# Kernel tuning notes

Measured on AMD Instinct MI355X. Metric: run time of the kernel, lower is better.

## Reference

```python
import jax, jax.numpy as jnp
import numpy as np

B, S, E, H = 8, 1024, 512, 8
NEG = -1e10


def setup_inputs() -> dict:
    key = jax.random.key(0)
    ks = jax.random.split(key, 8)
    k = jax.random.normal(ks[0], (B, S, E), dtype=jnp.float32)
    v = jax.random.normal(ks[1], (B, S, E), dtype=jnp.float32)
    q = jax.random.normal(ks[2], (B, S, E), dtype=jnp.float32)
    # causal mask, broadcastable like torch masked_fill
    mask = jnp.tril(jnp.ones((S, S), dtype=jnp.int32))[None, None]
    sc = 1.0 / np.sqrt(E)
    Wk = jax.random.normal(ks[3], (H * E, E), dtype=jnp.float32) * sc
    Wq = jax.random.normal(ks[4], (H * E, E), dtype=jnp.float32) * sc
    Wv = jax.random.normal(ks[5], (H * E, E), dtype=jnp.float32) * sc
    Wo = jax.random.normal(ks[6], (E, H * E), dtype=jnp.float32) * (1.0 / np.sqrt(H * E))
    bo = jnp.zeros((E,), dtype=jnp.float32)
    return {"k": k, "v": v, "q": q, "mask": mask,
            "Wk": Wk, "Wq": Wq, "Wv": Wv, "Wo": Wo, "bo": bo}


def reference(k, v, q, mask, Wk, Wq, Wv, Wo, bo):
    b, q_len, e = q.shape
    k_len, v_len = k.shape[1], v.shape[1]
    h = Wk.shape[0] // e
    scale = jnp.sqrt(jnp.asarray(e // h, dtype=jnp.float32))
    # projections E -> H*E (torch Linear: x @ W.T)
    wk = (k @ Wk.T).reshape(b, h, k_len, e)   # raw reshape, matches torch .view
    wq = (q @ Wq.T).reshape(b, h, q_len, e)
    wv = (v @ Wv.T).reshape(b, h, v_len, e)
    energy = jnp.einsum('bhqe,bhke->bhqk', wq, wk)
    energy = jnp.where(mask == 0, NEG, energy)  # mask applied BEFORE scaling, as in source
    energy = energy / scale
    attn = jax.nn.softmax(energy, axis=-1)
    f = jnp.einsum('bhqk,bhke->bhqe', attn, wv)
    f = jnp.transpose(f, (0, 2, 1, 3)).reshape(b, q_len, h * e)
    return f @ Wo.T + bo
```

## Files before the change

### kernel.cpp

```cpp
#include <hip/hip_runtime.h>


typedef _Float16 half8 __attribute__((ext_vector_type(8)));
typedef _Float16 half4v __attribute__((ext_vector_type(4)));
typedef float f32x4 __attribute__((ext_vector_type(4)));

typedef __attribute__((address_space(3))) unsigned int lds_u32_t;
typedef __attribute__((address_space(1))) unsigned int g_u32_t;

__device__ __forceinline__ void glds16(const void* g, void* l) {
  __builtin_amdgcn_global_load_lds((const g_u32_t*)g, (lds_u32_t*)l, 16, 0, 0);
}

__device__ __forceinline__ void stage_glds(const _Float16* tile, int ld, _Float16* lds) {
  int w = (int)threadIdx.x >> 6, lane = (int)threadIdx.x & 63;
  int row = lane >> 2, seg = (lane & 3) * 8;
  const _Float16* g0 = tile + (size_t)(w * 32 + row) * ld + seg;
  const _Float16* g1 = tile + (size_t)(w * 32 + 16 + row) * ld + seg;
  glds16(g0, lds + (size_t)(w * 32) * 32);
  glds16(g1, lds + (size_t)(w * 32 + 16) * 32);
}

template <int C3, int CMODE, bool CAUSAL, bool KLIM, int HL>
__global__ __launch_bounds__(256) void gemm_bt(
    const _Float16* __restrict__ Ap, const _Float16* __restrict__ Bp,
    void* __restrict__ C0, void* __restrict__ C1, void* __restrict__ C2,
    int tilesN, int K, int lda, int ldb, int ldc,
    long sAy, long sAz, long sAh, long sBy, long sBz, long sBh,
    long sCy, long sCz) {
  int i0 = ((int)blockIdx.x / tilesN) * 128;
  int j0 = ((int)blockIdx.x % tilesN) * 128;
  if (CAUSAL && j0 > i0) return;
  int Y = (int)blockIdx.y, Z = (int)blockIdx.z;
  const _Float16* Ab = Ap + (size_t)Y * sAy + (size_t)Z * sAz + (size_t)i0 * lda;
  const _Float16* Bb = Bp + (size_t)Y * sBy + (size_t)Z * sBz + (size_t)j0 * ldb;
  void* Cb = C3 ? (Y == 0 ? C0 : (Y == 1 ? C1 : C2)) : C0;
  size_t cOff = (C3 ? 0 : (size_t)Y * sCy) + (size_t)Z * sCz;

  __shared__ __align__(16) _Float16 As[128 * 32];
  __shared__ __align__(16) _Float16 Bs[128 * 32];

  int kmax = K;
  if (KLIM) { int kl = i0 + 128; kmax = kl < K ? kl : K; }

  int w = (int)threadIdx.x >> 6;
  int lane = (int)threadIdx.x & 63;
  int wr = (w >> 1) * 64, wc = (w & 1) * 64;
  int lr = lane & 15, lk = (lane >> 4) * 8;

  f32x4 acc[4][4] = {};

  for (int h = 0; h < HL; h++) {
    const _Float16* At = Ab + (size_t)h * sAh;
    const _Float16* Bt = Bb + (size_t)h * sBh;
    for (int k0 = 0; k0 < kmax; k0 += 32) {
      __syncthreads();
      stage_glds(At + k0, lda, As);
      stage_glds(Bt + k0, ldb, Bs);
      __syncthreads();

      half8 a[4], b[4];
#pragma unroll
      for (int mi = 0; mi < 4; mi++)
        a[mi] = *(half8*)&As[(wr + mi * 16 + lr) * 32 + lk];
#pragma unroll
      for (int ni = 0; ni < 4; ni++)
        b[ni] = *(half8*)&Bs[(wc + ni * 16 + lr) * 32 + lk];
#pragma unroll
      for (int mi = 0; mi < 4; mi++)
#pragma unroll
        for (int ni = 0; ni < 4; ni++)
          acc[mi][ni] = __builtin_amdgcn_mfma_f32_16x16x32_f16(a[mi], b[ni], acc[mi][ni], 0, 0, 0);
    }
  }

  int r0 = (lane >> 4) * 4, col = lane & 15;
#pragma unroll
  for (int mi = 0; mi < 4; mi++) {
#pragma unroll
    for (int ni = 0; ni < 4; ni++) {
      int gcol = j0 + wc + ni * 16 + col;
      int growb = i0 + wr + mi * 16 + r0;
#pragma unroll
      for (int r = 0; r < 4; r++) {
        size_t off = cOff + (size_t)(growb + r) * ldc + gcol;
        if (CMODE == 1)
          unsafeAtomicAdd((float*)Cb + off, acc[mi][ni][r]);
        else
          ((_Float16*)Cb)[off] = (_Float16)acc[mi][ni][r];
      }
    }
  }
}

__global__ __launch_bounds__(256) void softmax_rows(void* __restrict__ Ep) {
  int R = (int)blockIdx.x * 4 + ((int)threadIdx.x >> 6);
  int lane = (int)threadIdx.x & 63;
  int i = R & 1023;
  int nt = (i >> 8) + 1;
  _Float16* row = (_Float16*)Ep + (size_t)R * 1024;
  float x[16];
  float m = -3.0e38f;
#pragma unroll
  for (int t = 0; t < 4; t++) {
    if (t < nt) {
      int j0 = t * 256 + lane * 4;
      half4v h = *(const half4v*)(row + j0);
#pragma unroll
      for (int c = 0; c < 4; c++) {
        float v = (j0 + c <= i) ? (float)h[c] * 0.125f : -3.0e38f;
        x[t * 4 + c] = v;
        m = fmaxf(m, v);
      }
    }
  }
#pragma unroll
  for (int s = 32; s > 0; s >>= 1) m = fmaxf(m, __shfl_xor(m, s, 64));
  float p[16];
  float sum = 0.0f;
#pragma unroll
  for (int t = 0; t < 4; t++) {
    if (t < nt) {
#pragma unroll
      for (int c = 0; c < 4; c++) {
        p[t * 4 + c] = exp2f((x[t * 4 + c] - m) * 1.44269504f);
        sum += p[t * 4 + c];
      }
    }
  }
#pragma unroll
  for (int s = 32; s > 0; s >>= 1) sum += __shfl_xor(sum, s, 64);
  float inv = 1.0f / sum;
#pragma unroll
  for (int t = 0; t < 4; t++) {
    if (t < nt) {
      int j0 = t * 256 + lane * 4;
      half4v h;
#pragma unroll
      for (int c = 0; c < 4; c++) h[c] = (_Float16)(p[t * 4 + c] * inv);
      *(half4v*)(row + j0) = h;
    }
  }
}

__global__ __launch_bounds__(256) void wconv(const float* __restrict__ Wq,
                                             const float* __restrict__ Wk,
                                             const float* __restrict__ Wv,
                                             const float* __restrict__ Wo,
                                             _Float16* __restrict__ W16) {
  size_t base = ((size_t)blockIdx.x * 256 + threadIdx.x) * 8;
  int wid = (int)(base >> 21);
  size_t off = base & 2097151;
  const float* src = wid == 0 ? Wq : (wid == 1 ? Wk : (wid == 2 ? Wv : Wo));
  float4 a = *(const float4*)(src + off);
  float4 b = *(const float4*)(src + off + 4);
  half8 h;
  h[0] = (_Float16)a.x; h[1] = (_Float16)a.y; h[2] = (_Float16)a.z; h[3] = (_Float16)a.w;
  h[4] = (_Float16)b.x; h[5] = (_Float16)b.y; h[6] = (_Float16)b.z; h[7] = (_Float16)b.w;
  *(half8*)(W16 + base) = h;
}

template <int HG>
__global__ __launch_bounds__(256) void inconv(const float* __restrict__ q,
                                              const float* __restrict__ k,
                                              const float* __restrict__ v,
                                              _Float16* __restrict__ dst) {
  int Y = (int)blockIdx.y;
  size_t base = ((size_t)blockIdx.x * 256 + threadIdx.x) * 8;
  size_t b = base / (HG * 65536);
  size_t within = base - b * (HG * 65536);
  const float* src = (Y == 0 ? q : (Y == 1 ? k : v)) + b * 524288 + within;
  float4 a = ((const float4*)src)[0];
  float4 c = ((const float4*)src)[1];
  half8 h;
  h[0] = (_Float16)a.x; h[1] = (_Float16)a.y; h[2] = (_Float16)a.z; h[3] = (_Float16)a.w;
  h[4] = (_Float16)c.x; h[5] = (_Float16)c.y; h[6] = (_Float16)c.z; h[7] = (_Float16)c.w;
  *(half8*)(dst + (size_t)Y * HG * 524288 + base) = h;
}

__global__ __launch_bounds__(256) void bias_init(float* __restrict__ out,
                                                 const float* __restrict__ bo) {
  size_t idx = ((size_t)blockIdx.x * 256 + threadIdx.x) * 4;
  *(float4*)(out + idx) = *(const float4*)(bo + (idx & 511));
}

template <int HG>
static void run_pipeline(const float* q_in, const float* k_in, const float* v_in,
                         const float* Wq, const float* Wk, const float* Wv,
                         const float* Wo, const float* bo, float* out, char* ws,
                         hipStream_t stream) {
  const int NG = 8 / HG;
  const long zc = 8 * HG;
  _Float16* W16 = (_Float16*)ws;
  _Float16* in16 = W16 + 8388608;
  _Float16* Qp = in16 + 3L * HG * 524288;
  _Float16* Kp = Qp + zc * 524288;
  _Float16* VWo = Kp + zc * 524288;
  _Float16* E = VWo + zc * 524288;
  _Float16* Vp = E;
  _Float16* Wo16 = W16 + 3 * 2097152;
  dim3 blk(256);

  wconv<<<dim3(4096), blk, 0, stream>>>(Wq, Wk, Wv, Wo, W16);
  bias_init<<<dim3(4096), blk, 0, stream>>>(out, bo);

  constexpr int YS = (HG > 1) ? HG / 2 : 1;
  constexpr int HL = HG / YS;

  for (int g = 0; g < NG; g++) {
    inconv<HG><<<dim3(HG * 256, 3), blk, 0, stream>>>(
        q_in + (size_t)g * HG * 65536, k_in + (size_t)g * HG * 65536,
        v_in + (size_t)g * HG * 65536, in16);

    gemm_bt<1, 0, false, false, 1><<<dim3(HG * 32, 3, 8), blk, 0, stream>>>(
        in16, W16, Qp, Kp, Vp, 32, 512, 512, 512, 4096,
        (long)HG * 524288, (long)HG * 65536, 0, 2097152, 0, 0,
        0, (long)HG * 524288);

    gemm_bt<0, 0, false, false, 1><<<dim3(32, HG, 8), blk, 0, stream>>>(
        Wo16 + (size_t)g * HG * 512, Vp, VWo, nullptr, nullptr,
        8, 512, 4096, 512, 1024,
        512, 0, 0, 524288, (long)HG * 524288, 0,
        524288, (long)HG * 524288);

    gemm_bt<0, 0, true, false, 1><<<dim3(64, HG, 8), blk, 0, stream>>>(
        Qp, Kp, E, nullptr, nullptr, 8, 512, 512, 512, 1024,
        524288, (long)HG * 524288, 0, 524288, (long)HG * 524288, 0,
        1048576, (long)HG * 1048576);

    softmax_rows<<<dim3(zc * 256), blk, 0, stream>>>(E);

    gemm_bt<0, 1, false, true, HL><<<dim3(32, YS, 8), blk, 0, stream>>>(
        E, VWo, out, nullptr, nullptr, 4, 1024, 1024, 1024, 512,
        (long)HL * 1048576, (long)HG * 1048576, 1048576,
        (long)HL * 524288, (long)HG * 524288, 524288,
        0, 524288);
  }
}

extern "C" void kernel_launch(void* const* d_in, const int* in_sizes, int n_in,
                              void* d_out, int out_size, void* d_ws, size_t ws_size,
                              hipStream_t stream) {
  const float* k_in = (const float*)d_in[0];
  const float* v_in = (const float*)d_in[1];
  const float* q_in = (const float*)d_in[2];
  const float* Wk = (const float*)d_in[4];
  const float* Wq = (const float*)d_in[5];
  const float* Wv = (const float*)d_in[6];
  const float* Wo = (const float*)d_in[7];
  const float* bo = (const float*)d_in[8];
  float* out = (float*)d_out;
  char* ws = (char*)d_ws;

  if (ws_size >= (size_t)197132288)
    run_pipeline<4>(q_in, k_in, v_in, Wq, Wk, Wv, Wo, bo, out, ws, stream);
  else if (ws_size >= (size_t)106954752)
    run_pipeline<2>(q_in, k_in, v_in, Wq, Wk, Wv, Wo, bo, out, ws, stream);
  else
    run_pipeline<1>(q_in, k_in, v_in, Wq, Wk, Wv, Wo, bo, out, ws, stream);
}
```

Before: 632.0 us.

## Split GEMM into specialized kernels with BK=64, LDS-staged stores, triangular causal grid

The generic gemm_bt is replaced by per-stage kernels built on a shared core that stages 64-wide K slices per barrier pair instead of 32. The f16 outputs now go through an LDS transpose so each thread writes 16-byte rows. The energy GEMM launches only the 36 lower-triangular tiles, computed with a sqrt index mapping, instead of returning early from masked blocks. The weight and bias init kernels merge into one launch, and the PV head split changes to HL=2. These aim to cut barrier count, scattered 2-byte stores and idle blocks, at the cost of more LDS per block, which may reduce occupancy.

```diff
diff --git a/kernel.cpp b/kernel.cpp
--- a/kernel.cpp
+++ b/kernel.cpp
@@ -12,85 +12,161 @@
   __builtin_amdgcn_global_load_lds((const g_u32_t*)g, (lds_u32_t*)l, 16, 0, 0);
 }
 
-__device__ __forceinline__ void stage_glds(const _Float16* tile, int ld, _Float16* lds) {
-  int w = (int)threadIdx.x >> 6, lane = (int)threadIdx.x & 63;
-  int row = lane >> 2, seg = (lane & 3) * 8;
-  const _Float16* g0 = tile + (size_t)(w * 32 + row) * ld + seg;
-  const _Float16* g1 = tile + (size_t)(w * 32 + 16 + row) * ld + seg;
-  glds16(g0, lds + (size_t)(w * 32) * 32);
-  glds16(g1, lds + (size_t)(w * 32 + 16) * 32);
-}
-
-template <int C3, int CMODE, bool CAUSAL, bool KLIM, int HL>
-__global__ __launch_bounds__(256) void gemm_bt(
-    const _Float16* __restrict__ Ap, const _Float16* __restrict__ Bp,
-    void* __restrict__ C0, void* __restrict__ C1, void* __restrict__ C2,
-    int tilesN, int K, int lda, int ldb, int ldc,
-    long sAy, long sAz, long sAh, long sBy, long sBz, long sBh,
-    long sCy, long sCz) {
-  int i0 = ((int)blockIdx.x / tilesN) * 128;
-  int j0 = ((int)blockIdx.x % tilesN) * 128;
-  if (CAUSAL && j0 > i0) return;
-  int Y = (int)blockIdx.y, Z = (int)blockIdx.z;
-  const _Float16* Ab = Ap + (size_t)Y * sAy + (size_t)Z * sAz + (size_t)i0 * lda;
-  const _Float16* Bb = Bp + (size_t)Y * sBy + (size_t)Z * sBz + (size_t)j0 * ldb;
-  void* Cb = C3 ? (Y == 0 ? C0 : (Y == 1 ? C1 : C2)) : C0;
-  size_t cOff = (C3 ? 0 : (size_t)Y * sCy) + (size_t)Z * sCz;
-
-  __shared__ __align__(16) _Float16 As[128 * 32];
-  __shared__ __align__(16) _Float16 Bs[128 * 32];
-
-  int kmax = K;
-  if (KLIM) { int kl = i0 + 128; kmax = kl < K ? kl : K; }
-
-  int w = (int)threadIdx.x >> 6;
-  int lane = (int)threadIdx.x & 63;
+template <int HL>
+__device__ __forceinline__ void gemm_core(const _Float16* A, const _Float16* B,
+                                          int lda, int ldb, int kmax,
+                                          long sAh, long sBh,
+                                          _Float16* As, _Float16* Bs,
+                                          f32x4 (&acc)[4][4]) {
+  int tid = (int)threadIdx.x;
+  int w = tid >> 6, lane = tid & 63;
   int wr = (w >> 1) * 64, wc = (w & 1) * 64;
   int lr = lane & 15, lk = (lane >> 4) * 8;
-
-  f32x4 acc[4][4] = {};
+  int srow = lane >> 2, sseg = (lane & 3) * 8;
 
   for (int h = 0; h < HL; h++) {
-    const _Float16* At = Ab + (size_t)h * sAh;
-    const _Float16* Bt = Bb + (size_t)h * sBh;
-    for (int k0 = 0; k0 < kmax; k0 += 32) {
+    const _Float16* Ah = A + (size_t)h * sAh;
+    const _Float16* Bh = B + (size_t)h * sBh;
+    for (int k0 = 0; k0 < kmax; k0 += 64) {
       __syncthreads();
-      stage_glds(At + k0, lda, As);
-      stage_glds(Bt + k0, ldb, Bs);
+#pragma unroll
+      for (int p = 0; p < 2; p++)
+#pragma unroll
+        for (int t = 0; t < 2; t++) {
+          glds16(Ah + (size_t)(w * 32 + t * 16 + srow) * lda + k0 + p * 32 + sseg,
+                 As + p * 4096 + (w * 32 + t * 16) * 32);
+          glds16(Bh + (size_t)(w * 32 + t * 16 + srow) * ldb + k0 + p * 32 + sseg,
+                 Bs + p * 4096 + (w * 32 + t * 16) * 32);
+        }
       __syncthreads();
-
-      half8 a[4], b[4];
-#pragma unroll
-      for (int mi = 0; mi < 4; mi++)
-        a[mi] = *(half8*)&As[(wr + mi * 16 + lr) * 32 + lk];
-#pragma unroll
-      for (int ni = 0; ni < 4; ni++)
-        b[ni] = *(half8*)&Bs[(wc + ni * 16 + lr) * 32 + lk];
-#pragma unroll
-      for (int mi = 0; mi < 4; mi++)
+#pragma unroll
+      for (int p = 0; p < 2; p++) {
+        half8 a[4], b[4];
+#pragma unroll
+        for (int mi = 0; mi < 4; mi++)
+          a[mi] = *(half8*)&As[p * 4096 + (wr + mi * 16 + lr) * 32 + lk];
 #pragma unroll
         for (int ni = 0; ni < 4; ni++)
-          acc[mi][ni] = __builtin_amdgcn_mfma_f32_16x16x32_f16(a[mi], b[ni], acc[mi][ni], 0, 0, 0);
-    }
-  }
-
-  int r0 = (lane >> 4) * 4, col = lane & 15;
-#pragma unroll
-  for (int mi = 0; mi < 4; mi++) {
-#pragma unroll
-    for (int ni = 0; ni < 4; ni++) {
-      int gcol = j0 + wc + ni * 16 + col;
-      int growb = i0 + wr + mi * 16 + r0;
-#pragma unroll
-      for (int r = 0; r < 4; r++) {
-        size_t off = cOff + (size_t)(growb + r) * ldc + gcol;
-        if (CMODE == 1)
-          unsafeAtomicAdd((float*)Cb + off, acc[mi][ni][r]);
-        else
-          ((_Float16*)Cb)[off] = (_Float16)acc[mi][ni][r];
+          b[ni] = *(half8*)&Bs[p * 4096 + (wc + ni * 16 + lr) * 32 + lk];
+#pragma unroll
+        for (int mi = 0; mi < 4; mi++)
+#pragma unroll
+          for (int ni = 0; ni < 4; ni++)
+            acc[mi][ni] =
+                __builtin_amdgcn_mfma_f32_16x16x32_f16(a[mi], b[ni], acc[mi][ni], 0, 0, 0);
       }
     }
   }
+}
+
+__device__ __forceinline__ void epilogue_f16(f32x4 (&acc)[4][4], _Float16* T,
+                                             _Float16* Cp, size_t cOff,
+                                             int i0, int j0, int ldc) {
+  int tid = (int)threadIdx.x;
+  int w = tid >> 6, lane = tid & 63;
+  int wr = (w >> 1) * 64, wc = (w & 1) * 64;
+  int r0 = (lane >> 4) * 4, col = lane & 15;
+  __syncthreads();
+#pragma unroll
+  for (int mi = 0; mi < 4; mi++)
+#pragma unroll
+    for (int ni = 0; ni < 4; ni++)
+#pragma unroll
+      for (int r = 0; r < 4; r++)
+        T[(size_t)(wr + mi * 16 + r0 + r) * 136 + wc + ni * 16 + col] =
+            (_Float16)acc[mi][ni][r];
+  __syncthreads();
+#pragma unroll
+  for (int s = 0; s < 8; s++) {
+    int row = w * 32 + s * 4 + (lane >> 4);
+    int c8 = (lane & 15) * 8;
+    half8 h = *(half8*)&T[(size_t)row * 136 + c8];
+    *(half8*)(Cp + cOff + (size_t)(i0 + row) * ldc + j0 + c8) = h;
+  }
+}
+
+__device__ __forceinline__ void epilogue_atomic(f32x4 (&acc)[4][4], float* Cp,
+                                                size_t cOff, int i0, int j0, int ldc) {
+  int tid = (int)threadIdx.x;
+  int w = tid >> 6, lane = tid & 63;
+  int wr = (w >> 1) * 64, wc = (w & 1) * 64;
+  int r0 = (lane >> 4) * 4, col = lane & 15;
+#pragma unroll
+  for (int mi = 0; mi < 4; mi++)
+#pragma unroll
+    for (int ni = 0; ni < 4; ni++)
+#pragma unroll
+      for (int r = 0; r < 4; r++)
+        unsafeAtomicAdd(Cp + cOff + (size_t)(i0 + wr + mi * 16 + r0 + r) * ldc +
+                            j0 + wc + ni * 16 + col,
+                        acc[mi][ni][r]);
+}
+
+template <int HG>
+__global__ __launch_bounds__(256) void proj_kernel(const _Float16* __restrict__ in16,
+                                                   const _Float16* __restrict__ W16,
+                                                   _Float16* __restrict__ Qp,
+                                                   _Float16* __restrict__ Kp,
+                                                   _Float16* __restrict__ Vp) {
+  __shared__ __align__(16) _Float16 smem[17408];
+  int x = (int)blockIdx.x, Y = (int)blockIdx.y, Z = (int)blockIdx.z;
+  int i0 = (x >> 5) * 128, j0 = (x & 31) * 128;
+  const _Float16* A = in16 + (size_t)Y * HG * 524288 + (size_t)Z * HG * 65536 +
+                      (size_t)i0 * 512;
+  const _Float16* B = W16 + (size_t)Y * 2097152 + (size_t)j0 * 512;
+  _Float16* C = (Y == 0 ? Qp : (Y == 1 ? Kp : Vp));
+  f32x4 acc[4][4] = {};
+  gemm_core<1>(A, B, 512, 512, 512, 0, 0, smem, smem + 8192, acc);
+  epilogue_f16(acc, smem, C, (size_t)Z * HG * 524288, i0, j0, 4096);
+}
+
+template <int HG>
+__global__ __launch_bounds__(256) void vwo_kernel(const _Float16* __restrict__ Vp,
+                                                  const _Float16* __restrict__ WoG,
+                                                  _Float16* __restrict__ VWo) {
+  __shared__ __align__(16) _Float16 smem[17408];
+  int x = (int)blockIdx.x, Y = (int)blockIdx.y, Z = (int)blockIdx.z;
+  size_t z = (size_t)Z * HG + Y;
+  int i0 = (x >> 3) * 128, j0 = (x & 7) * 128;
+  const _Float16* A = WoG + (size_t)Y * 512 + (size_t)i0 * 4096;
+  const _Float16* B = Vp + z * 524288 + (size_t)j0 * 512;
+  f32x4 acc[4][4] = {};
+  gemm_core<1>(A, B, 4096, 512, 512, 0, 0, smem, smem + 8192, acc);
+  epilogue_f16(acc, smem, VWo, z * 524288, i0, j0, 1024);
+}
+
+template <int HG>
+__global__ __launch_bounds__(256) void energy_kernel(const _Float16* __restrict__ Qp,
+                                                     const _Float16* __restrict__ Kp,
+                                                     _Float16* __restrict__ E) {
+  __shared__ __align__(16) _Float16 smem[17408];
+  int x = (int)blockIdx.x, Y = (int)blockIdx.y, Z = (int)blockIdx.z;
+  size_t z = (size_t)Z * HG + Y;
+  int ti = (int)((sqrtf(8.0f * x + 1.0f) - 1.0f) * 0.5f);
+  if (ti * (ti + 1) / 2 > x) ti--;
+  else if ((ti + 1) * (ti + 2) / 2 <= x) ti++;
+  int tj = x - ti * (ti + 1) / 2;
+  int i0 = ti * 128, j0 = tj * 128;
+  const _Float16* A = Qp + z * 524288 + (size_t)i0 * 512;
+  const _Float16* B = Kp + z * 524288 + (size_t)j0 * 512;
+  f32x4 acc[4][4] = {};
+  gemm_core<1>(A, B, 512, 512, 512, 0, 0, smem, smem + 8192, acc);
+  epilogue_f16(acc, smem, E, z * 1048576, i0, j0, 1024);
+}
+
+template <int HG, int HL>
+__global__ __launch_bounds__(256) void pv_kernel(const _Float16* __restrict__ E,
+                                                 const _Float16* __restrict__ VWo,
+                                                 float* __restrict__ out) {
+  __shared__ __align__(16) _Float16 smem[17408];
+  int x = (int)blockIdx.x, Y = (int)blockIdx.y, Z = (int)blockIdx.z;
+  int i0 = (x >> 2) * 128, j0 = (x & 3) * 128;
+  int kmax = i0 + 128;
+  const _Float16* A = E + ((size_t)Z * HG + (size_t)Y * HL) * 1048576 + (size_t)i0 * 1024;
+  const _Float16* B = VWo + ((size_t)Z * HG + (size_t)Y * HL) * 524288 + (size_t)j0 * 1024;
+  f32x4 acc[4][4] = {};
+  gemm_core<HL>(A, B, 1024, 1024, kmax, 1048576, 524288, smem, smem + 8192, acc);
+  epilogue_atomic(acc, out, (size_t)Z * 524288, i0, j0, 512);
 }
 
 __global__ __launch_bounds__(256) void softmax_rows(void* __restrict__ Ep) {
@@ -143,21 +219,29 @@
   }
 }
 
-__global__ __launch_bounds__(256) void wconv(const float* __restrict__ Wq,
-                                             const float* __restrict__ Wk,
-                                             const float* __restrict__ Wv,
-                                             const float* __restrict__ Wo,
-                                             _Float16* __restrict__ W16) {
-  size_t base = ((size_t)blockIdx.x * 256 + threadIdx.x) * 8;
-  int wid = (int)(base >> 21);
-  size_t off = base & 2097151;
-  const float* src = wid == 0 ? Wq : (wid == 1 ? Wk : (wid == 2 ? Wv : Wo));
-  float4 a = *(const float4*)(src + off);
-  float4 b = *(const float4*)(src + off + 4);
-  half8 h;
-  h[0] = (_Float16)a.x; h[1] = (_Float16)a.y; h[2] = (_Float16)a.z; h[3] = (_Float16)a.w;
-  h[4] = (_Float16)b.x; h[5] = (_Float16)b.y; h[6] = (_Float16)b.z; h[7] = (_Float16)b.w;
-  *(half8*)(W16 + base) = h;
+__global__ __launch_bounds__(256) void wbconv(const float* __restrict__ Wq,
+                                              const float* __restrict__ Wk,
+                                              const float* __restrict__ Wv,
+                                              const float* __restrict__ Wo,
+                                              _Float16* __restrict__ W16,
+                                              float* __restrict__ out,
+                                              const float* __restrict__ bo) {
+  int bx = (int)blockIdx.x;
+  if (bx < 4096) {
+    size_t base = ((size_t)bx * 256 + threadIdx.x) * 8;
+    int wid = (int)(base >> 21);
+    size_t off = base & 2097151;
+    const float* src = wid == 0 ? Wq : (wid == 1 ? Wk : (wid == 2 ? Wv : Wo));
+    float4 a = *(const float4*)(src + off);
+    float4 b = *(const float4*)(src + off + 4);
+    half8 h;
+    h[0] = (_Float16)a.x; h[1] = (_Float16)a.y; h[2] = (_Float16)a.z; h[3] = (_Float16)a.w;
+    h[4] = (_Float16)b.x; h[5] = (_Float16)b.y; h[6] = (_Float16)b.z; h[7] = (_Float16)b.w;
+    *(half8*)(W16 + base) = h;
+  } else {
+    size_t idx = ((size_t)(bx - 4096) * 256 + threadIdx.x) * 4;
+    *(float4*)(out + idx) = *(const float4*)(bo + (idx & 511));
+  }
 }
 
 template <int HG>
@@ -178,12 +262,6 @@
   *(half8*)(dst + (size_t)Y * HG * 524288 + base) = h;
 }
 
-__global__ __launch_bounds__(256) void bias_init(float* __restrict__ out,
-                                                 const float* __restrict__ bo) {
-  size_t idx = ((size_t)blockIdx.x * 256 + threadIdx.x) * 4;
-  *(float4*)(out + idx) = *(const float4*)(bo + (idx & 511));
-}
-
 template <int HG>
 static void run_pipeline(const float* q_in, const float* k_in, const float* v_in,
                          const float* Wq, const float* Wk, const float* Wv,
@@ -201,40 +279,26 @@
   _Float16* Wo16 = W16 + 3 * 2097152;
   dim3 blk(256);
 
-  wconv<<<dim3(4096), blk, 0, stream>>>(Wq, Wk, Wv, Wo, W16);
-  bias_init<<<dim3(4096), blk, 0, stream>>>(out, bo);
-
-  constexpr int YS = (HG > 1) ? HG / 2 : 1;
-  constexpr int HL = HG / YS;
+  wbconv<<<dim3(8192), blk, 0, stream>>>(Wq, Wk, Wv, Wo, W16, out, bo);
+
+  constexpr int HL = (HG >= 2) ? 2 : 1;
+  constexpr int YS = HG / HL;
 
   for (int g = 0; g < NG; g++) {
     inconv<HG><<<dim3(HG * 256, 3), blk, 0, stream>>>(
         q_in + (size_t)g * HG * 65536, k_in + (size_t)g * HG * 65536,
         v_in + (size_t)g * HG * 65536, in16);
 
-    gemm_bt<1, 0, false, false, 1><<<dim3(HG * 32, 3, 8), blk, 0, stream>>>(
-        in16, W16, Qp, Kp, Vp, 32, 512, 512, 512, 4096,
-        (long)HG * 524288, (long)HG * 65536, 0, 2097152, 0, 0,
-        0, (long)HG * 524288);
-
-    gemm_bt<0, 0, false, false, 1><<<dim3(32, HG, 8), blk, 0, stream>>>(
-        Wo16 + (size_t)g * HG * 512, Vp, VWo, nullptr, nullptr,
-        8, 512, 4096, 512, 1024,
-        512, 0, 0, 524288, (long)HG * 524288, 0,
-        524288, (long)HG * 524288);
-
-    gemm_bt<0, 0, true, false, 1><<<dim3(64, HG, 8), blk, 0, stream>>>(
-        Qp, Kp, E, nullptr, nullptr, 8, 512, 512, 512, 1024,
-        524288, (long)HG * 524288, 0, 524288, (long)HG * 524288, 0,
-        1048576, (long)HG * 1048576);
+    proj_kernel<HG><<<dim3(HG * 32, 3, 8), blk, 0, stream>>>(in16, W16, Qp, Kp, Vp);
+
+    vwo_kernel<HG><<<dim3(32, HG, 8), blk, 0, stream>>>(
+        Vp, Wo16 + (size_t)g * HG * 512, VWo);
+
+    energy_kernel<HG><<<dim3(36, HG, 8), blk, 0, stream>>>(Qp, Kp, E);
 
     softmax_rows<<<dim3(zc * 256), blk, 0, stream>>>(E);
 
-    gemm_bt<0, 1, false, true, HL><<<dim3(32, YS, 8), blk, 0, stream>>>(
-        E, VWo, out, nullptr, nullptr, 4, 1024, 1024, 1024, 512,
-        (long)HL * 1048576, (long)HG * 1048576, 1048576,
-        (long)HL * 524288, (long)HG * 524288, 524288,
-        0, 524288);
+    pv_kernel<HG, HL><<<dim3(32, YS, 8), blk, 0, stream>>>(E, VWo, out);
   }
 }
 
```

Measured after the change: 572.3 us. -9.5%, faster.
